# Kernel optimization log

Measured on AMD Instinct MI355X. Metric: run time of the kernel, lower is better.

## Reference

```python
import jax, jax.numpy as jnp
import numpy as np

B, C, H, W = 16, 256, 64, 64
K = 1024

def setup_inputs() -> dict:
    key = jax.random.key(0)
    k1, k2 = jax.random.split(key)
    x = jax.random.normal(k1, (B, C, H, W), dtype=jnp.float32)
    codebook = jax.random.normal(k2, (K, C), dtype=jnp.float32)
    return {"x": x, "codebook": codebook}


def reference(x, codebook):
    b, c, h, w = x.shape
    # (B, C, H, W) -> (B*H*W, C)
    xf = jnp.transpose(x, (0, 2, 3, 1)).reshape(-1, c)
    # Squared euclidean distances to codebook (argmin is the same as for cdist).
    x2 = jnp.sum(xf * xf, axis=-1, keepdims=True)          # (N, 1)
    c2 = jnp.sum(codebook * codebook, axis=-1)               # (K,)
    dist = x2 - 2.0 * jnp.einsum('nc,kc->nk', xf, codebook) + c2  # (N, K)
    idx = jnp.argmin(dist, axis=-1)                          # (N,)
    quant = codebook[idx]                                     # (N, C)
    commitment_loss = jnp.mean((jax.lax.stop_gradient(quant) - xf) ** 2)
    codebook_loss = jnp.mean((quant - jax.lax.stop_gradient(xf)) ** 2)
    # Straight-through estimator
    quant_out = xf + jax.lax.stop_gradient(quant - xf)
    quant_out = jnp.transpose(quant_out.reshape(b, h, w, c), (0, 3, 1, 2))
    indices = idx.reshape(b, h, w)
    return quant_out, codebook_loss, commitment_loss, indices
```

## Files before the change

### kernel.cpp

```cpp
#include <hip/hip_runtime.h>

constexpr int Bn = 16, Cd = 256, Hn = 64, Wn = 64, Kc = 1024;
constexpr int QUANT_ELEMS = Bn * Hn * Wn * Cd;
constexpr int LOSS_OFF = QUANT_ELEMS;
constexpr int IDX_OFF = QUANT_ELEMS + 2;

typedef _Float16 half8 __attribute__((ext_vector_type(8)));
typedef float f32x4 __attribute__((ext_vector_type(4)));

constexpr size_t WS_CBFH = 0;
constexpr size_t WS_CBFL = 512 * 1024;
constexpr size_t WS_C2   = 1024 * 1024;

constexpr float THR = 1e-4f;

static __device__ __forceinline__ float med3f(float a, float b, float c) {
#if __has_builtin(__builtin_amdgcn_fmed3f)
    return __builtin_amdgcn_fmed3f(a, b, c);
#else
    return fmaxf(fminf(a, b), fminf(fmaxf(a, b), c));
#endif
}

__global__ __launch_bounds__(256) void prep(const float* __restrict__ cb,
                                            _Float16* __restrict__ cbFh,
                                            _Float16* __restrict__ cbFl,
                                            float* __restrict__ c2,
                                            float* __restrict__ out) {
    __shared__ float cbs[16][257];
    const int tid = threadIdx.x;
    const int k0 = blockIdx.x * 16;
    {
        const int c4 = (tid & 63) * 4;
        const int r0 = tid >> 6;
        #pragma unroll
        for (int it = 0; it < 4; ++it) {
            const int r = r0 + it * 4;
            const float4 v = *(const float4*)&cb[(size_t)(k0 + r) * Cd + c4];
            cbs[r][c4] = v.x; cbs[r][c4 + 1] = v.y; cbs[r][c4 + 2] = v.z; cbs[r][c4 + 3] = v.w;
        }
    }
    __syncthreads();
    {
        const int i = tid >> 4, part = tid & 15;
        float s = 0.f;
        #pragma unroll
        for (int c = part * 16; c < part * 16 + 16; ++c) { const float v = cbs[i][c]; s += v * v; }
        s += __shfl_xor(s, 1);
        s += __shfl_xor(s, 2);
        s += __shfl_xor(s, 4);
        s += __shfl_xor(s, 8);
        if (part == 0) c2[k0 + i] = s;
    }
    for (int t = tid; t < 512; t += 256) {
        const int kblk = t >> 6;
        const int l = t & 63;
        const int code_l = l & 15;
        const int cbase = kblk * 32 + (l >> 4) * 8;
        half8 hv, lv;
        #pragma unroll
        for (int j = 0; j < 8; ++j) {
            const float v = cbs[code_l][cbase + j];
            const _Float16 hh = (_Float16)v;
            hv[j] = hh;
            lv[j] = (_Float16)(v - (float)hh);
        }
        const size_t e = (size_t)(blockIdx.x * 8 + kblk) * 64 + l;
        *(half8*)(cbFh + e * 8) = hv;
        *(half8*)(cbFl + e * 8) = lv;
    }
    if (blockIdx.x == 0 && tid == 0) {
        out[LOSS_OFF] = 0.f; out[LOSS_OFF + 1] = 0.f;
    }
}

__global__ __launch_bounds__(512, 4) void vq_main(const float* __restrict__ x,
                                                  const _Float16* __restrict__ cbFh,
                                                  const _Float16* __restrict__ cbFl,
                                                  const float* __restrict__ c2,
                                                  const float* __restrict__ cb,
                                                  float* __restrict__ out) {
    __shared__ half8 Axh[2048];
    __shared__ half8 Axl[2048];
    __shared__ float q1ds[8][32];
    __shared__ int   q1is[8][32];
    __shared__ float q2ds[8][32];
    __shared__ int   idx_s[64];
    __shared__ float red[8];
    __shared__ int   flg[64];
    __shared__ int   nflag;
    __shared__ float scan_xs[256];
    __shared__ float scan_d[8];
    __shared__ int   scan_k[8];

    const int tid = threadIdx.x;
    const int lane = tid & 63;
    const int wv = tid >> 6;
    const int mth = wv & 1;
    const int ntq = wv >> 1;
    const int bh = blockIdx.x;
    const int b = bh >> 6, h = bh & 63;

    if (tid == 0) nflag = 0;

    {
        const int m = tid & 15;
        const int q = (tid >> 4) & 3;
        const int mtg = (tid >> 6) & 3;
        const int kh = tid >> 8;
        const int w = mtg * 16 + m;
        const float* xb = x + ((size_t)b * Cd * Hn + h) * Wn + w;
        #pragma unroll
        for (int kk = 0; kk < 4; ++kk) {
            const int kblk = kh * 4 + kk;
            half8 hv, lv;
            #pragma unroll
            for (int j = 0; j < 8; ++j) {
                const int c = kblk * 32 + q * 8 + j;
                const float v = xb[(size_t)c * (Hn * Wn)];
                const _Float16 hh = (_Float16)v;
                hv[j] = hh;
                lv[j] = (_Float16)(v - (float)hh);
            }
            const int e = (kblk * 4 + mtg) * 64 + (q * 16 + m);
            Axh[e] = hv;
            Axl[e] = lv;
        }
    }
    __syncthreads();

    float q1d[8], q2d[8];
    int   q1i[8];
    #pragma unroll
    for (int i = 0; i < 8; ++i) { q1d[i] = 3.4e38f; q2d[i] = 3.4e38f; q1i[i] = 0; }

    half8 nbh[2], nbl[2];
    #pragma unroll
    for (int nt = 0; nt < 2; ++nt) {
        const int ntile = ntq * 16 + nt;
        const size_t be = ((size_t)(ntile * 8) * 64 + lane) * 8;
        nbh[nt] = *(const half8*)(cbFh + be);
        nbl[nt] = *(const half8*)(cbFl + be);
    }

    #pragma unroll 1
    for (int grp = 0; grp < 8; ++grp) {
        f32x4 acc[2][2];
        acc[0][0] = (f32x4){0.f, 0.f, 0.f, 0.f};
        acc[0][1] = (f32x4){0.f, 0.f, 0.f, 0.f};
        acc[1][0] = (f32x4){0.f, 0.f, 0.f, 0.f};
        acc[1][1] = (f32x4){0.f, 0.f, 0.f, 0.f};

        #pragma unroll 2
        for (int kblk = 0; kblk < 8; ++kblk) {
            const half8 cbh0 = nbh[0], cbh1 = nbh[1];
            const half8 cbl0 = nbl[0], cbl1 = nbl[1];
            {
                const int nk = (kblk + 1) & 7;
                const int ng = (grp + ((kblk + 1) >> 3)) & 7;
                #pragma unroll
                for (int nt = 0; nt < 2; ++nt) {
                    const int ntile = ntq * 16 + ng * 2 + nt;
                    const size_t be = ((size_t)(ntile * 8 + nk) * 64 + lane) * 8;
                    nbh[nt] = *(const half8*)(cbFh + be);
                    nbl[nt] = *(const half8*)(cbFl + be);
                }
            }
            half8 ahf[2], alf[2];
            #pragma unroll
            for (int ml = 0; ml < 2; ++ml) {
                const int e = (kblk * 4 + mth * 2 + ml) * 64 + lane;
                ahf[ml] = Axh[e];
                alf[ml] = Axl[e];
            }
            __builtin_amdgcn_s_setprio(1);
            #pragma unroll
            for (int ml = 0; ml < 2; ++ml) {
                acc[ml][0] = __builtin_amdgcn_mfma_f32_16x16x32_f16(ahf[ml], cbh0, acc[ml][0], 0, 0, 0);
                acc[ml][1] = __builtin_amdgcn_mfma_f32_16x16x32_f16(ahf[ml], cbh1, acc[ml][1], 0, 0, 0);
            }
            #pragma unroll
            for (int ml = 0; ml < 2; ++ml) {
                acc[ml][0] = __builtin_amdgcn_mfma_f32_16x16x32_f16(ahf[ml], cbl0, acc[ml][0], 0, 0, 0);
                acc[ml][1] = __builtin_amdgcn_mfma_f32_16x16x32_f16(ahf[ml], cbl1, acc[ml][1], 0, 0, 0);
            }
            #pragma unroll
            for (int ml = 0; ml < 2; ++ml) {
                acc[ml][0] = __builtin_amdgcn_mfma_f32_16x16x32_f16(alf[ml], cbh0, acc[ml][0], 0, 0, 0);
                acc[ml][1] = __builtin_amdgcn_mfma_f32_16x16x32_f16(alf[ml], cbh1, acc[ml][1], 0, 0, 0);
            }
            __builtin_amdgcn_s_setprio(0);
        }

        #pragma unroll
        for (int nt = 0; nt < 2; ++nt) {
            const int code = (ntq * 16 + grp * 2 + nt) * 16 + (lane & 15);
            const float c2v = c2[code];
            #pragma unroll
            for (int ml = 0; ml < 2; ++ml) {
                #pragma unroll
                for (int reg = 0; reg < 4; ++reg) {
                    const float d = fmaf(-2.f, acc[ml][nt][reg], c2v);
                    const int qi = ml * 4 + reg;
                    q2d[qi] = med3f(q1d[qi], q2d[qi], d);
                    q1i[qi] = (d < q1d[qi]) ? code : q1i[qi];
                    q1d[qi] = fminf(q1d[qi], d);
                }
            }
        }
    }

    #pragma unroll
    for (int off = 1; off < 16; off <<= 1) {
        #pragma unroll
        for (int qi = 0; qi < 8; ++qi) {
            const float od1 = __shfl_xor(q1d[qi], off);
            const int   oi1 = __shfl_xor(q1i[qi], off);
            const float od2 = __shfl_xor(q2d[qi], off);
            const float hi = fmaxf(q1d[qi], od1);
            q2d[qi] = fminf(fminf(q2d[qi], od2), hi);
            q1i[qi] = (od1 < q1d[qi]) ? oi1 : q1i[qi];
            q1d[qi] = fminf(q1d[qi], od1);
        }
    }
    if ((lane & 15) == 0) {
        #pragma unroll
        for (int qi = 0; qi < 8; ++qi) {
            const int ml = qi >> 2, reg = qi & 3;
            const int rl = ml * 16 + (lane >> 4) * 4 + reg;
            q1ds[wv][rl] = q1d[qi];
            q1is[wv][rl] = q1i[qi];
            q2ds[wv][rl] = q2d[qi];
        }
    }
    __syncthreads();
    if (tid < 64) {
        const int hh = tid >> 5, rl = tid & 31;
        float d1 = q1ds[hh][rl]; int i1 = q1is[hh][rl]; float d2 = q2ds[hh][rl];
        #pragma unroll
        for (int v = 1; v < 4; ++v) {
            const int w2 = hh + 2 * v;
            const float od1 = q1ds[w2][rl]; const int oi1 = q1is[w2][rl];
            const float od2 = q2ds[w2][rl];
            const float hi = fmaxf(d1, od1);
            d2 = fminf(fminf(d2, od2), hi);
            i1 = (od1 < d1) ? oi1 : i1;
            d1 = fminf(d1, od1);
        }
        idx_s[tid] = i1;
        if (d2 - d1 < THR) {
            const int pos = atomicAdd(&nflag, 1);
            flg[pos] = tid;
        }
    }
    __syncthreads();

    const int nf = nflag;
    for (int fi = 0; fi < nf; ++fi) {
        const int wrow = flg[fi];
        if (tid < 256) {
            const int c = tid;
            const int mt = wrow >> 4, m = wrow & 15;
            const int e = ((c >> 5) * 4 + mt) * 64 + ((c >> 3) & 3) * 16 + m;
            const int j = c & 7;
            scan_xs[c] = (float)Axh[e][j] + (float)Axl[e][j];
        }
        __syncthreads();
        float bd = 3.4e38f; int bk = 0;
        #pragma unroll
        for (int r = 0; r < 2; ++r) {
            const int code = tid * 2 + r;
            const float4* cr = (const float4*)(cb + (size_t)code * Cd);
            const float4* xr = (const float4*)scan_xs;
            float dot = 0.f;
            #pragma unroll 8
            for (int i = 0; i < 64; ++i) {
                const float4 v = cr[i];
                const float4 xv = xr[i];
                dot = fmaf(v.x, xv.x, dot);
                dot = fmaf(v.y, xv.y, dot);
                dot = fmaf(v.z, xv.z, dot);
                dot = fmaf(v.w, xv.w, dot);
            }
            const float d = c2[code] - 2.f * dot;
            if (d < bd || (d == bd && code < bk)) { bd = d; bk = code; }
        }
        #pragma unroll
        for (int off = 32; off >= 1; off >>= 1) {
            const float od = __shfl_xor(bd, off);
            const int   ok = __shfl_xor(bk, off);
            if (od < bd || (od == bd && ok < bk)) { bd = od; bk = ok; }
        }
        if (lane == 0) { scan_d[wv] = bd; scan_k[wv] = bk; }
        __syncthreads();
        if (tid == 0) {
            float fd = scan_d[0]; int fk = scan_k[0];
            #pragma unroll
            for (int v = 1; v < 8; ++v) {
                const float od = scan_d[v]; const int ok = scan_k[v];
                if (od < fd || (od == fd && ok < fk)) { fd = od; fk = ok; }
            }
            idx_s[wrow] = fk;
        }
        __syncthreads();
    }

    if (tid < 64) out[IDX_OFF + bh * 64 + tid] = (float)idx_s[tid];

    {
        const int w = tid & 63;
        const int kblk = wv;
        const int m = w & 15, mt = w >> 4;
        const int myidx = idx_s[w];
        const float4* cbrow = (const float4*)(cb + (size_t)myidx * Cd + kblk * 32);
        float lsum = 0.f;
        #pragma unroll
        for (int q = 0; q < 4; ++q) {
            const int e = (kblk * 4 + mt) * 64 + q * 16 + m;
            const half8 hv = Axh[e];
            const half8 lv = Axl[e];
            const float4 qa = cbrow[q * 2];
            const float4 qb = cbrow[q * 2 + 1];
            const float qv[8] = {qa.x, qa.y, qa.z, qa.w, qb.x, qb.y, qb.z, qb.w};
            const int cbase = kblk * 32 + q * 8;
            #pragma unroll
            for (int j = 0; j < 8; ++j) {
                const float xv = (float)hv[j] + (float)lv[j];
                const float dd = qv[j] - xv;
                lsum += dd * dd;
                out[(((size_t)b * Cd + cbase + j) * Hn + h) * Wn + w] = qv[j];
            }
        }
        #pragma unroll
        for (int off = 32; off >= 1; off >>= 1) lsum += __shfl_xor(lsum, off);
        if (lane == 0) red[wv] = lsum;
    }
    __syncthreads();
    if (tid == 0) {
        float s = 0.f;
        #pragma unroll
        for (int i = 0; i < 8; ++i) s += red[i];
        s *= (1.0f / 16777216.0f);
        atomicAdd(out + LOSS_OFF, s);
        atomicAdd(out + LOSS_OFF + 1, s);
    }
}

extern "C" void kernel_launch(void* const* d_in, const int* in_sizes, int n_in,
                              void* d_out, int out_size, void* d_ws, size_t ws_size,
                              hipStream_t stream) {
    const float* x  = (const float*)d_in[0];
    const float* cb = (const float*)d_in[1];
    float* out = (float*)d_out;
    char* ws = (char*)d_ws;
    _Float16* cbFh = (_Float16*)(ws + WS_CBFH);
    _Float16* cbFl = (_Float16*)(ws + WS_CBFL);
    float* c2      = (float*)(ws + WS_C2);

    prep<<<64, 256, 0, stream>>>(cb, cbFh, cbFl, c2, out);
    vq_main<<<Bn * Hn, 512, 0, stream>>>(x, cbFh, cbFl, c2, cb, out);
}
```

Before: 214.0 us.

## Fuse codebook prep into main kernel via cooperative grid sync

```diff
diff --git a/kernel.cpp b/kernel.cpp
--- a/kernel.cpp
+++ b/kernel.cpp
@@ -1,4 +1,7 @@
 #include <hip/hip_runtime.h>
+#include <hip/hip_cooperative_groups.h>
+
+namespace cg = cooperative_groups;
 
 constexpr int Bn = 16, Cd = 256, Hn = 64, Wn = 64, Kc = 1024;
 constexpr int QUANT_ELEMS = Bn * Hn * Wn * Cd;
@@ -22,64 +25,12 @@
 #endif
 }
 
-__global__ __launch_bounds__(256) void prep(const float* __restrict__ cb,
-                                            _Float16* __restrict__ cbFh,
-                                            _Float16* __restrict__ cbFl,
-                                            float* __restrict__ c2,
-                                            float* __restrict__ out) {
-    __shared__ float cbs[16][257];
-    const int tid = threadIdx.x;
-    const int k0 = blockIdx.x * 16;
-    {
-        const int c4 = (tid & 63) * 4;
-        const int r0 = tid >> 6;
-        #pragma unroll
-        for (int it = 0; it < 4; ++it) {
-            const int r = r0 + it * 4;
-            const float4 v = *(const float4*)&cb[(size_t)(k0 + r) * Cd + c4];
-            cbs[r][c4] = v.x; cbs[r][c4 + 1] = v.y; cbs[r][c4 + 2] = v.z; cbs[r][c4 + 3] = v.w;
-        }
-    }
-    __syncthreads();
-    {
-        const int i = tid >> 4, part = tid & 15;
-        float s = 0.f;
-        #pragma unroll
-        for (int c = part * 16; c < part * 16 + 16; ++c) { const float v = cbs[i][c]; s += v * v; }
-        s += __shfl_xor(s, 1);
-        s += __shfl_xor(s, 2);
-        s += __shfl_xor(s, 4);
-        s += __shfl_xor(s, 8);
-        if (part == 0) c2[k0 + i] = s;
-    }
-    for (int t = tid; t < 512; t += 256) {
-        const int kblk = t >> 6;
-        const int l = t & 63;
-        const int code_l = l & 15;
-        const int cbase = kblk * 32 + (l >> 4) * 8;
-        half8 hv, lv;
-        #pragma unroll
-        for (int j = 0; j < 8; ++j) {
-            const float v = cbs[code_l][cbase + j];
-            const _Float16 hh = (_Float16)v;
-            hv[j] = hh;
-            lv[j] = (_Float16)(v - (float)hh);
-        }
-        const size_t e = (size_t)(blockIdx.x * 8 + kblk) * 64 + l;
-        *(half8*)(cbFh + e * 8) = hv;
-        *(half8*)(cbFl + e * 8) = lv;
-    }
-    if (blockIdx.x == 0 && tid == 0) {
-        out[LOSS_OFF] = 0.f; out[LOSS_OFF + 1] = 0.f;
-    }
-}
-
-__global__ __launch_bounds__(512, 4) void vq_main(const float* __restrict__ x,
-                                                  const _Float16* __restrict__ cbFh,
-                                                  const _Float16* __restrict__ cbFl,
-                                                  const float* __restrict__ c2,
-                                                  const float* __restrict__ cb,
-                                                  float* __restrict__ out) {
+__global__ __launch_bounds__(512, 4) void vq_fused(const float* __restrict__ x,
+                                                   const float* __restrict__ cb,
+                                                   _Float16* __restrict__ cbFh,
+                                                   _Float16* __restrict__ cbFl,
+                                                   float* __restrict__ c2,
+                                                   float* __restrict__ out) {
     __shared__ half8 Axh[2048];
     __shared__ half8 Axl[2048];
     __shared__ float q1ds[8][32];
@@ -98,11 +49,369 @@
     const int wv = tid >> 6;
     const int mth = wv & 1;
     const int ntq = wv >> 1;
+
+    {
+        const int unit = blockIdx.x;
+        const int ntile = unit >> 3, kblk = unit & 7;
+        const int code_r = tid >> 5;
+        const int cc = tid & 31;
+        const float v = cb[(size_t)(ntile * 16 + code_r) * Cd + kblk * 32 + cc];
+        const _Float16 hh = (_Float16)v;
+        const _Float16 ll = (_Float16)(v - (float)hh);
+        const int l = ((cc >> 3) << 4) | code_r;
+        const int j = cc & 7;
+        const size_t e = (size_t)(ntile * 8 + kblk) * 64 + l;
+        cbFh[e * 8 + j] = hh;
+        cbFl[e * 8 + j] = ll;
+        if (kblk == 0) {
+            const int i = tid >> 5, part = tid & 31;
+            const float* row = cb + (size_t)(ntile * 16 + i) * Cd;
+            float s = 0.f;
+            #pragma unroll
+            for (int c0 = 0; c0 < 8; ++c0) { const float vv = row[part * 8 + c0]; s += vv * vv; }
+            s += __shfl_xor(s, 1);
+            s += __shfl_xor(s, 2);
+            s += __shfl_xor(s, 4);
+            s += __shfl_xor(s, 8);
+            s += __shfl_xor(s, 16);
+            if (part == 0) c2[ntile * 16 + i] = s;
+        }
+        if (unit == 0 && tid == 0) { out[LOSS_OFF] = 0.f; out[LOSS_OFF + 1] = 0.f; }
+    }
+    __threadfence();
+    cg::this_grid().sync();
+
+    #pragma unroll 1
+    for (int tt = 0; tt < 2; ++tt) {
+        const int bh = blockIdx.x * 2 + tt;
+        const int b = bh >> 6, h = bh & 63;
+
+        if (tid == 0) nflag = 0;
+
+        {
+            const int m = tid & 15;
+            const int q = (tid >> 4) & 3;
+            const int mtg = (tid >> 6) & 3;
+            const int kh = tid >> 8;
+            const int w = mtg * 16 + m;
+            const float* xb = x + ((size_t)b * Cd * Hn + h) * Wn + w;
+            #pragma unroll
+            for (int kk = 0; kk < 4; ++kk) {
+                const int kblk = kh * 4 + kk;
+                half8 hv, lv;
+                #pragma unroll
+                for (int j = 0; j < 8; ++j) {
+                    const int c = kblk * 32 + q * 8 + j;
+                    const float v = xb[(size_t)c * (Hn * Wn)];
+                    const _Float16 hh = (_Float16)v;
+                    hv[j] = hh;
+                    lv[j] = (_Float16)(v - (float)hh);
+                }
+                const int e = (kblk * 4 + mtg) * 64 + (q * 16 + m);
+                Axh[e] = hv;
+                Axl[e] = lv;
+            }
+        }
+        __syncthreads();
+
+        float q1d[8], q2d[8];
+        int   q1i[8];
+        #pragma unroll
+        for (int i = 0; i < 8; ++i) { q1d[i] = 3.4e38f; q2d[i] = 3.4e38f; q1i[i] = 0; }
+
+        half8 nbh[2], nbl[2];
+        #pragma unroll
+        for (int nt = 0; nt < 2; ++nt) {
+            const int ntile = ntq * 16 + nt;
+            const size_t be = ((size_t)(ntile * 8) * 64 + lane) * 8;
+            nbh[nt] = *(const half8*)(cbFh + be);
+            nbl[nt] = *(const half8*)(cbFl + be);
+        }
+
+        #pragma unroll 1
+        for (int grp = 0; grp < 8; ++grp) {
+            f32x4 acc[2][2];
+            acc[0][0] = (f32x4){0.f, 0.f, 0.f, 0.f};
+            acc[0][1] = (f32x4){0.f, 0.f, 0.f, 0.f};
+            acc[1][0] = (f32x4){0.f, 0.f, 0.f, 0.f};
+            acc[1][1] = (f32x4){0.f, 0.f, 0.f, 0.f};
+
+            #pragma unroll 2
+            for (int kblk = 0; kblk < 8; ++kblk) {
+                const half8 cbh0 = nbh[0], cbh1 = nbh[1];
+                const half8 cbl0 = nbl[0], cbl1 = nbl[1];
+                {
+                    const int nk = (kblk + 1) & 7;
+                    const int ng = (grp + ((kblk + 1) >> 3)) & 7;
+                    #pragma unroll
+                    for (int nt = 0; nt < 2; ++nt) {
+                        const int ntile = ntq * 16 + ng * 2 + nt;
+                        const size_t be = ((size_t)(ntile * 8 + nk) * 64 + lane) * 8;
+                        nbh[nt] = *(const half8*)(cbFh + be);
+                        nbl[nt] = *(const half8*)(cbFl + be);
+                    }
+                }
+                half8 ahf[2], alf[2];
+                #pragma unroll
+                for (int ml = 0; ml < 2; ++ml) {
+                    const int e = (kblk * 4 + mth * 2 + ml) * 64 + lane;
+                    ahf[ml] = Axh[e];
+                    alf[ml] = Axl[e];
+                }
+                __builtin_amdgcn_s_setprio(1);
+                #pragma unroll
+                for (int ml = 0; ml < 2; ++ml) {
+                    acc[ml][0] = __builtin_amdgcn_mfma_f32_16x16x32_f16(ahf[ml], cbh0, acc[ml][0], 0, 0, 0);
+                    acc[ml][1] = __builtin_amdgcn_mfma_f32_16x16x32_f16(ahf[ml], cbh1, acc[ml][1], 0, 0, 0);
+                }
+                #pragma unroll
+                for (int ml = 0; ml < 2; ++ml) {
+                    acc[ml][0] = __builtin_amdgcn_mfma_f32_16x16x32_f16(ahf[ml], cbl0, acc[ml][0], 0, 0, 0);
+                    acc[ml][1] = __builtin_amdgcn_mfma_f32_16x16x32_f16(ahf[ml], cbl1, acc[ml][1], 0, 0, 0);
+                }
+                #pragma unroll
+                for (int ml = 0; ml < 2; ++ml) {
+                    acc[ml][0] = __builtin_amdgcn_mfma_f32_16x16x32_f16(alf[ml], cbh0, acc[ml][0], 0, 0, 0);
+                    acc[ml][1] = __builtin_amdgcn_mfma_f32_16x16x32_f16(alf[ml], cbh1, acc[ml][1], 0, 0, 0);
+                }
+                __builtin_amdgcn_s_setprio(0);
+            }
+
+            #pragma unroll
+            for (int nt = 0; nt < 2; ++nt) {
+                const int code = (ntq * 16 + grp * 2 + nt) * 16 + (lane & 15);
+                const float c2v = c2[code];
+                #pragma unroll
+                for (int ml = 0; ml < 2; ++ml) {
+                    #pragma unroll
+                    for (int reg = 0; reg < 4; ++reg) {
+                        const float d = fmaf(-2.f, acc[ml][nt][reg], c2v);
+                        const int qi = ml * 4 + reg;
+                        q2d[qi] = med3f(q1d[qi], q2d[qi], d);
+                        q1i[qi] = (d < q1d[qi]) ? code : q1i[qi];
+                        q1d[qi] = fminf(q1d[qi], d);
+                    }
+                }
+            }
+        }
+
+        #pragma unroll
+        for (int off = 1; off < 16; off <<= 1) {
+            #pragma unroll
+            for (int qi = 0; qi < 8; ++qi) {
+                const float od1 = __shfl_xor(q1d[qi], off);
+                const int   oi1 = __shfl_xor(q1i[qi], off);
+                const float od2 = __shfl_xor(q2d[qi], off);
+                const float hi = fmaxf(q1d[qi], od1);
+                q2d[qi] = fminf(fminf(q2d[qi], od2), hi);
+                q1i[qi] = (od1 < q1d[qi]) ? oi1 : q1i[qi];
+                q1d[qi] = fminf(q1d[qi], od1);
+            }
+        }
+        if ((lane & 15) == 0) {
+            #pragma unroll
+            for (int qi = 0; qi < 8; ++qi) {
+                const int ml = qi >> 2, reg = qi & 3;
+                const int rl = ml * 16 + (lane >> 4) * 4 + reg;
+                q1ds[wv][rl] = q1d[qi];
+                q1is[wv][rl] = q1i[qi];
+                q2ds[wv][rl] = q2d[qi];
+            }
+        }
+        __syncthreads();
+        if (tid < 64) {
+            const int hh = tid >> 5, rl = tid & 31;
+            float d1 = q1ds[hh][rl]; int i1 = q1is[hh][rl]; float d2 = q2ds[hh][rl];
+            #pragma unroll
+            for (int v = 1; v < 4; ++v) {
+                const int w2 = hh + 2 * v;
+                const float od1 = q1ds[w2][rl]; const int oi1 = q1is[w2][rl];
+                const float od2 = q2ds[w2][rl];
+                const float hi = fmaxf(d1, od1);
+                d2 = fminf(fminf(d2, od2), hi);
+                i1 = (od1 < d1) ? oi1 : i1;
+                d1 = fminf(d1, od1);
+            }
+            idx_s[tid] = i1;
+            if (d2 - d1 < THR) {
+                const int pos = atomicAdd(&nflag, 1);
+                flg[pos] = tid;
+            }
+        }
+        __syncthreads();
+
+        const int nf = nflag;
+        for (int fi = 0; fi < nf; ++fi) {
+            const int wrow = flg[fi];
+            if (tid < 256) {
+                const int c = tid;
+                const int mt = wrow >> 4, m = wrow & 15;
+                const int e = ((c >> 5) * 4 + mt) * 64 + ((c >> 3) & 3) * 16 + m;
+                const int j = c & 7;
+                scan_xs[c] = (float)Axh[e][j] + (float)Axl[e][j];
+            }
+            __syncthreads();
+            float bd = 3.4e38f; int bk = 0;
+            #pragma unroll
+            for (int r = 0; r < 2; ++r) {
+                const int code = tid * 2 + r;
+                const float4* cr = (const float4*)(cb + (size_t)code * Cd);
+                const float4* xr = (const float4*)scan_xs;
+                float dot = 0.f;
+                #pragma unroll 8
+                for (int i = 0; i < 64; ++i) {
+                    const float4 v = cr[i];
+                    const float4 xv = xr[i];
+                    dot = fmaf(v.x, xv.x, dot);
+                    dot = fmaf(v.y, xv.y, dot);
+                    dot = fmaf(v.z, xv.z, dot);
+                    dot = fmaf(v.w, xv.w, dot);
+                }
+                const float d = c2[code] - 2.f * dot;
+                if (d < bd || (d == bd && code < bk)) { bd = d; bk = code; }
+            }
+            #pragma unroll
+            for (int off = 32; off >= 1; off >>= 1) {
+                const float od = __shfl_xor(bd, off);
+                const int   ok = __shfl_xor(bk, off);
+                if (od < bd || (od == bd && ok < bk)) { bd = od; bk = ok; }
+            }
+            if (lane == 0) { scan_d[wv] = bd; scan_k[wv] = bk; }
+            __syncthreads();
+            if (tid == 0) {
+                float fd = scan_d[0]; int fk = scan_k[0];
+                #pragma unroll
+                for (int v = 1; v < 8; ++v) {
+                    const float od = scan_d[v]; const int ok = scan_k[v];
+                    if (od < fd || (od == fd && ok < fk)) { fd = od; fk = ok; }
+                }
+                idx_s[wrow] = fk;
+            }
+            __syncthreads();
+        }
+
+        if (tid < 64) out[IDX_OFF + bh * 64 + tid] = (float)idx_s[tid];
+
+        {
+            const int w = tid & 63;
+            const int kblk = wv;
+            const int m = w & 15, mt = w >> 4;
+            const int myidx = idx_s[w];
+            const float4* cbrow = (const float4*)(cb + (size_t)myidx * Cd + kblk * 32);
+            float lsum = 0.f;
+            #pragma unroll
+            for (int q = 0; q < 4; ++q) {
+                const int e = (kblk * 4 + mt) * 64 + q * 16 + m;
+                const half8 hv = Axh[e];
+                const half8 lv = Axl[e];
+                const float4 qa = cbrow[q * 2];
+                const float4 qb = cbrow[q * 2 + 1];
+                const float qv[8] = {qa.x, qa.y, qa.z, qa.w, qb.x, qb.y, qb.z, qb.w};
+                const int cbase = kblk * 32 + q * 8;
+                #pragma unroll
+                for (int j = 0; j < 8; ++j) {
+                    const float xv = (float)hv[j] + (float)lv[j];
+                    const float dd = qv[j] - xv;
+                    lsum += dd * dd;
+                    out[(((size_t)b * Cd + cbase + j) * Hn + h) * Wn + w] = qv[j];
+                }
+            }
+            #pragma unroll
+            for (int off = 32; off >= 1; off >>= 1) lsum += __shfl_xor(lsum, off);
+            if (lane == 0) red[wv] = lsum;
+        }
+        __syncthreads();
+        if (tid == 0) {
+            float s = 0.f;
+            #pragma unroll
+            for (int i = 0; i < 8; ++i) s += red[i];
+            s *= (1.0f / 16777216.0f);
+            atomicAdd(out + LOSS_OFF, s);
+            atomicAdd(out + LOSS_OFF + 1, s);
+        }
+    }
+}
+
+__global__ __launch_bounds__(256) void prep(const float* __restrict__ cb,
+                                            _Float16* __restrict__ cbFh,
+                                            _Float16* __restrict__ cbFl,
+                                            float* __restrict__ c2,
+                                            float* __restrict__ out) {
+    __shared__ float cbs[16][257];
+    const int tid = threadIdx.x;
+    const int k0 = blockIdx.x * 16;
+    {
+        const int c4 = (tid & 63) * 4;
+        const int r0 = tid >> 6;
+        #pragma unroll
+        for (int it = 0; it < 4; ++it) {
+            const int r = r0 + it * 4;
+            const float4 v = *(const float4*)&cb[(size_t)(k0 + r) * Cd + c4];
+            cbs[r][c4] = v.x; cbs[r][c4 + 1] = v.y; cbs[r][c4 + 2] = v.z; cbs[r][c4 + 3] = v.w;
+        }
+    }
+    __syncthreads();
+    {
+        const int i = tid >> 4, part = tid & 15;
+        float s = 0.f;
+        #pragma unroll
+        for (int c = part * 16; c < part * 16 + 16; ++c) { const float v = cbs[i][c]; s += v * v; }
+        s += __shfl_xor(s, 1);
+        s += __shfl_xor(s, 2);
+        s += __shfl_xor(s, 4);
+        s += __shfl_xor(s, 8);
+        if (part == 0) c2[k0 + i] = s;
+    }
+    for (int t = tid; t < 512; t += 256) {
+        const int kblk = t >> 6;
+        const int l = t & 63;
+        const int code_l = l & 15;
+        const int cbase = kblk * 32 + (l >> 4) * 8;
+        half8 hv, lv;
+        #pragma unroll
+        for (int j = 0; j < 8; ++j) {
+            const float v = cbs[code_l][cbase + j];
+            const _Float16 hh = (_Float16)v;
+            hv[j] = hh;
+            lv[j] = (_Float16)(v - (float)hh);
+        }
+        const size_t e = (size_t)(blockIdx.x * 8 + kblk) * 64 + l;
+        *(half8*)(cbFh + e * 8) = hv;
+        *(half8*)(cbFl + e * 8) = lv;
+    }
+    if (blockIdx.x == 0 && tid == 0) {
+        out[LOSS_OFF] = 0.f; out[LOSS_OFF + 1] = 0.f;
+    }
+}
+
+__global__ __launch_bounds__(512, 4) void vq_main_fb(const float* __restrict__ x,
+                                                     const float* __restrict__ cb,
+                                                     const _Float16* __restrict__ cbFh,
+                                                     const _Float16* __restrict__ cbFl,
+                                                     const float* __restrict__ c2,
+                                                     float* __restrict__ out) {
+    __shared__ half8 Axh[2048];
+    __shared__ half8 Axl[2048];
+    __shared__ float q1ds[8][32];
+    __shared__ int   q1is[8][32];
+    __shared__ float q2ds[8][32];
+    __shared__ int   idx_s[64];
+    __shared__ float red[8];
+    __shared__ int   flg[64];
+    __shared__ int   nflag;
+    __shared__ float scan_xs[256];
+    __shared__ float scan_d[8];
+    __shared__ int   scan_k[8];
+
+    const int tid = threadIdx.x;
+    const int lane = tid & 63;
+    const int wv = tid >> 6;
+    const int mth = wv & 1;
+    const int ntq = wv >> 1;
     const int bh = blockIdx.x;
     const int b = bh >> 6, h = bh & 63;
 
     if (tid == 0) nflag = 0;
-
     {
         const int m = tid & 15;
         const int q = (tid >> 4) & 3;
@@ -357,6 +666,12 @@
     _Float16* cbFl = (_Float16*)(ws + WS_CBFL);
     float* c2      = (float*)(ws + WS_C2);
 
-    prep<<<64, 256, 0, stream>>>(cb, cbFh, cbFl, c2, out);
-    vq_main<<<Bn * Hn, 512, 0, stream>>>(x, cbFh, cbFl, c2, cb, out);
+    void* args[] = {(void*)&x, (void*)&cb, (void*)&cbFh, (void*)&cbFl,
+                    (void*)&c2, (void*)&out};
+    const hipError_t err = hipLaunchCooperativeKernel(
+        (const void*)vq_fused, dim3(512), dim3(512), args, 0, stream);
+    if (err != hipSuccess) {
+        prep<<<64, 256, 0, stream>>>(cb, cbFh, cbFl, c2, out);
+        vq_main_fb<<<Bn * Hn, 512, 0, stream>>>(x, cb, cbFh, cbFl, c2, out);
+    }
 }
```

Result: slower. 350.0 us (+63.6%).
